# Kernel optimization log

Hardware: AMD Instinct MI355X
Metric: run time of the kernel (lower is better)

Reference implementation:

```python
import jax, jax.numpy as jnp
import numpy as np

N_ITERATIONS = 3  # matches init_kwargs n_iterations


def squash(s):
    # s: [batch, output_caps, output_dim]
    sq = jnp.sum(s * s, axis=2, keepdims=True)          # [b, oc, 1]
    return s * (sq / (1.0 + sq) / jnp.sqrt(sq))


def setup_inputs() -> dict:
    key = jax.random.key(0)
    k_u, = jax.random.split(key, 1)
    batch, ic, oc, od = 128, 2048, 32, 16
    u_predict = jax.random.normal(k_u, (batch, ic, oc, od), dtype=jnp.float32)
    b = jnp.zeros((ic, oc), dtype=jnp.float32)  # routing logit prior, init zeros per torch module
    return {"u_predict": u_predict, "b": b}


def reference(u_predict, b):
    # u_predict: [batch, input_caps, output_caps, output_dim]; b: [input_caps, output_caps]
    batch = u_predict.shape[0]
    c = jax.nn.softmax(b, axis=1)                              # softmax over output_caps (torch implicit dim=1 on 2D)
    s = jnp.einsum('io,biod->bod', c, u_predict)               # weighted sum over input_caps
    v = squash(s)
    b_batch = jnp.broadcast_to(b, (batch,) + b.shape)          # [b, ic, oc]
    for _ in range(N_ITERATIONS):
        b_batch = b_batch + jnp.einsum('biod,bod->bio', u_predict, v)  # agreement
        c = jax.nn.softmax(b_batch, axis=-1)                   # coupling coeffs over output_caps
        s = jnp.einsum('bio,biod->bod', c, u_predict)
        v = squash(s)
    return v
```

## Files before the change

### kernel.cpp

```cpp
#include <hip/hip_runtime.h>
#include <math.h>


namespace {
constexpr int BATCH = 128;
constexpr int IC    = 2048;
constexpr int OC    = 32;
constexpr int ROW   = 512;
constexpr int BPB   = 16;
constexpr int ROWS_PER_BLOCK = IC / BPB;
constexpr int NWAVES = 4;
constexpr int HROW  = ROW / 8;

typedef _Float16 half8 __attribute__((ext_vector_type(8)));
typedef float    f32x4 __attribute__((ext_vector_type(4)));

constexpr size_t OFF_U16    = 0;
constexpr size_t PART_BYTES = (size_t)BATCH * BPB * ROW * 4;
constexpr size_t OFF_P0     = 268435456;
constexpr size_t OFF_P1     = OFF_P0 + PART_BYTES;
constexpr size_t OFF_WA     = OFF_P1 + PART_BYTES;
constexpr size_t OFF_WB     = OFF_WA + 262144;
}

__global__ void __launch_bounds__(256)
pass0_convert(const float* __restrict__ u, const float* __restrict__ blogit,
              _Float16* __restrict__ u16, float* __restrict__ partials)
{
    const int tid = threadIdx.x, lane = tid & 63, wave = tid >> 6;
    const int b = blockIdx.x >> 4, chunk = blockIdx.x & 15;
    const int o = lane >> 1, elem0 = lane * 8;
    const int i_base = chunk * ROWS_PER_BLOCK + wave * 32;

    f32x4 acc0 = {0.f,0.f,0.f,0.f}, acc1 = {0.f,0.f,0.f,0.f};

    const float*  ubase = u   + ((size_t)b * IC + i_base) * ROW + elem0;
    _Float16*     obase = u16 + ((size_t)b * IC + i_base) * ROW + elem0;

#pragma unroll 4
    for (int r = 0; r < 32; ++r) {
        const float* up = ubase + (size_t)r * ROW;
        f32x4 u0 = __builtin_nontemporal_load((const f32x4*)up);
        f32x4 u1 = __builtin_nontemporal_load((const f32x4*)(up + 4));
        float e = __expf(blogit[(i_base + r) * OC + o]);
        float ssum = e;
#pragma unroll
        for (int off = 2; off <= 32; off <<= 1)
            ssum += __shfl_xor(ssum, off, 64);
        const float c = e / ssum;
        acc0 += c * u0;
        acc1 += c * u1;
        half8 h;
        h[0]=(_Float16)u0[0]; h[1]=(_Float16)u0[1]; h[2]=(_Float16)u0[2]; h[3]=(_Float16)u0[3];
        h[4]=(_Float16)u1[0]; h[5]=(_Float16)u1[1]; h[6]=(_Float16)u1[2]; h[7]=(_Float16)u1[3];
        __builtin_nontemporal_store(h, (half8*)(obase + (size_t)r * ROW));
    }

    __shared__ float red[NWAVES * ROW];
    float* my = red + wave * ROW + elem0;
    *(f32x4*)my       = acc0;
    *(f32x4*)(my + 4) = acc1;
    __syncthreads();
    float* dst = partials + (size_t)blockIdx.x * ROW;
    for (int p = tid; p < ROW; p += 256)
        dst[p] = red[p] + red[ROW + p] + red[2*ROW + p] + red[3*ROW + p];
}

template<int IT>
__device__ __forceinline__ void compute_w(const float* __restrict__ part_in,
                                          const float* __restrict__ w_in,
                                          float* __restrict__ w_out,
                                          float* __restrict__ wlds,
                                          int b, int tid, int chunk)
{
    const int p = tid * 2;
    const float* pp = part_in + (size_t)b * (BPB * ROW) + p;
    float s0 = 0.f, s1 = 0.f;
#pragma unroll
    for (int k = 0; k < BPB; ++k) {
        s0 += pp[(size_t)k * ROW];
        s1 += pp[(size_t)k * ROW + 1];
    }
    float sq = s0 * s0 + s1 * s1;
    sq += __shfl_xor(sq, 1, 64);
    sq += __shfl_xor(sq, 2, 64);
    sq += __shfl_xor(sq, 4, 64);
    const float sc = sqrtf(sq) / (1.0f + sq);
    float w0 = s0 * sc, w1 = s1 * sc;
    if (IT > 1) {
        w0 += w_in[b * ROW + p];
        w1 += w_in[b * ROW + p + 1];
    }
    wlds[p]     = w0;
    wlds[p + 1] = w1;
    if (IT < 3 && chunk == 0) {
        w_out[b * ROW + p]     = w0;
        w_out[b * ROW + p + 1] = w1;
    }
}

template<int IT>
__global__ void __launch_bounds__(256)
pass_iter(const _Float16* __restrict__ u16, const float* __restrict__ blogit,
          const float* __restrict__ part_in, const float* __restrict__ w_in,
          float* __restrict__ part_out, float* __restrict__ w_out)
{
    const int tid = threadIdx.x, lane = tid & 63, wave = tid >> 6;
    const int b = blockIdx.x >> 4, chunk = blockIdx.x & 15;
    const int o = lane >> 1, elem0 = lane * 8;
    const int i_base = chunk * ROWS_PER_BLOCK + wave * 32;

    __shared__ float red[NWAVES * ROW];
    __shared__ float wlds[ROW];

    const half8* ubase = (const half8*)(u16 + ((size_t)b * IC + i_base) * ROW + elem0);

    half8 cur[4];
    cur[0] = ubase[0*HROW]; cur[1] = ubase[1*HROW];
    cur[2] = ubase[2*HROW]; cur[3] = ubase[3*HROW];

    compute_w<IT>(part_in, w_in, w_out, wlds, b, tid, chunk);
    __syncthreads();

    const f32x4 w0 = *(const f32x4*)(wlds + elem0);
    const f32x4 w1 = *(const f32x4*)(wlds + elem0 + 4);

    f32x4 acc0 = {0.f,0.f,0.f,0.f}, acc1 = {0.f,0.f,0.f,0.f};

    for (int g = 0; g < 8; ++g) {
        half8 nxt[4];
        if (g < 7) {
            const half8* ptr = ubase + (size_t)(g + 1) * 4 * HROW;
            nxt[0] = ptr[0*HROW]; nxt[1] = ptr[1*HROW];
            nxt[2] = ptr[2*HROW]; nxt[3] = ptr[3*HROW];
        }
        float blg[4];
#pragma unroll
        for (int r = 0; r < 4; ++r)
            blg[r] = blogit[(i_base + g*4 + r) * OC + o];

#pragma unroll
        for (int r = 0; r < 4; ++r) {
            float uf[8];
#pragma unroll
            for (int j = 0; j < 8; ++j) uf[j] = (float)cur[r][j];
            float part = uf[0]*w0[0] + uf[1]*w0[1] + uf[2]*w0[2] + uf[3]*w0[3]
                       + uf[4]*w1[0] + uf[5]*w1[1] + uf[6]*w1[2] + uf[7]*w1[3];
            float bb = blg[r] + part + __shfl_xor(part, 1, 64);
            float e = __expf(bb);
            float ssum = e;
#pragma unroll
            for (int off = 2; off <= 32; off <<= 1)
                ssum += __shfl_xor(ssum, off, 64);
            const float c = e / ssum;
            acc0[0] += c*uf[0]; acc0[1] += c*uf[1]; acc0[2] += c*uf[2]; acc0[3] += c*uf[3];
            acc1[0] += c*uf[4]; acc1[1] += c*uf[5]; acc1[2] += c*uf[6]; acc1[3] += c*uf[7];
        }
#pragma unroll
        for (int r = 0; r < 4; ++r) cur[r] = nxt[r];
    }

    float* my = red + wave * ROW + elem0;
    *(f32x4*)my       = acc0;
    *(f32x4*)(my + 4) = acc1;
    __syncthreads();
    float* dst = part_out + (size_t)blockIdx.x * ROW;
    for (int p = tid; p < ROW; p += 256)
        dst[p] = red[p] + red[ROW + p] + red[2*ROW + p] + red[3*ROW + p];
}

__global__ void __launch_bounds__(256)
reduce_out(const float* __restrict__ partials, float* __restrict__ out)
{
    const int idx = blockIdx.x * 256 + threadIdx.x;
    const int b = idx >> 9, p = idx & 511;
    const float* pp = partials + (size_t)(b * BPB) * ROW + p;
    float s = 0.f;
#pragma unroll
    for (int k = 0; k < BPB; ++k) s += pp[(size_t)k * ROW];
    float sq = s * s;
    sq += __shfl_xor(sq, 1, 64);
    sq += __shfl_xor(sq, 2, 64);
    sq += __shfl_xor(sq, 4, 64);
    sq += __shfl_xor(sq, 8, 64);
    out[idx] = s * (sqrtf(sq) / (1.0f + sq));
}

extern "C" void kernel_launch(void* const* d_in, const int* in_sizes, int n_in,
                              void* d_out, int out_size, void* d_ws, size_t ws_size,
                              hipStream_t stream)
{
    const float* u  = (const float*)d_in[0];
    const float* bl = (const float*)d_in[1];
    float* out = (float*)d_out;

    char* ws = (char*)d_ws;
    _Float16* u16 = (_Float16*)(ws + OFF_U16);
    float* part0  = (float*)(ws + OFF_P0);
    float* part1  = (float*)(ws + OFF_P1);
    float* wA     = (float*)(ws + OFF_WA);
    float* wB     = (float*)(ws + OFF_WB);

    const dim3 blk(256);
    const dim3 gpass(BATCH * BPB);

    pass0_convert<<<gpass, blk, 0, stream>>>(u, bl, u16, part0);
    pass_iter<1> <<<gpass, blk, 0, stream>>>(u16, bl, part0, nullptr, part1, wA);
    pass_iter<2> <<<gpass, blk, 0, stream>>>(u16, bl, part1, wA,      part0, wB);
    pass_iter<3> <<<gpass, blk, 0, stream>>>(u16, bl, part0, wB,      part1, nullptr);
    reduce_out   <<<dim3(BATCH * ROW / 256), blk, 0, stream>>>(part1, out);
}
```

Before: 871.0 us.

## Split batch into halves so fp16 copy of u stays cache-resident across passes

The whole pipeline now runs twice, each time over half the batch (64 samples), and the fp16 conversion store becomes a normal cached store instead of a nontemporal one. The aim is for each half's fp16 working set (about 134 MB) to stay in the large last-level cache, so the three routing passes re-read it from cache rather than HBM. The cost is twice as many kernel launches, each with half the grid (1024 blocks), which may reduce occupancy and add launch and tail overhead.

```diff
diff --git a/kernel.cpp b/kernel.cpp
--- a/kernel.cpp
+++ b/kernel.cpp
@@ -4,6 +4,7 @@
 
 namespace {
 constexpr int BATCH = 128;
+constexpr int BHALF = 64;
 constexpr int IC    = 2048;
 constexpr int OC    = 32;
 constexpr int ROW   = 512;
@@ -25,10 +26,10 @@
 
 __global__ void __launch_bounds__(256)
 pass0_convert(const float* __restrict__ u, const float* __restrict__ blogit,
-              _Float16* __restrict__ u16, float* __restrict__ partials)
+              _Float16* __restrict__ u16, float* __restrict__ partials, int b0)
 {
     const int tid = threadIdx.x, lane = tid & 63, wave = tid >> 6;
-    const int b = blockIdx.x >> 4, chunk = blockIdx.x & 15;
+    const int b = b0 + (blockIdx.x >> 4), chunk = blockIdx.x & 15;
     const int o = lane >> 1, elem0 = lane * 8;
     const int i_base = chunk * ROWS_PER_BLOCK + wave * 32;
 
@@ -53,7 +54,7 @@
         half8 h;
         h[0]=(_Float16)u0[0]; h[1]=(_Float16)u0[1]; h[2]=(_Float16)u0[2]; h[3]=(_Float16)u0[3];
         h[4]=(_Float16)u1[0]; h[5]=(_Float16)u1[1]; h[6]=(_Float16)u1[2]; h[7]=(_Float16)u1[3];
-        __builtin_nontemporal_store(h, (half8*)(obase + (size_t)r * ROW));
+        *(half8*)(obase + (size_t)r * ROW) = h;
     }
 
     __shared__ float red[NWAVES * ROW];
@@ -61,7 +62,7 @@
     *(f32x4*)my       = acc0;
     *(f32x4*)(my + 4) = acc1;
     __syncthreads();
-    float* dst = partials + (size_t)blockIdx.x * ROW;
+    float* dst = partials + ((size_t)b * BPB + chunk) * ROW;
     for (int p = tid; p < ROW; p += 256)
         dst[p] = red[p] + red[ROW + p] + red[2*ROW + p] + red[3*ROW + p];
 }
@@ -103,10 +104,10 @@
 __global__ void __launch_bounds__(256)
 pass_iter(const _Float16* __restrict__ u16, const float* __restrict__ blogit,
           const float* __restrict__ part_in, const float* __restrict__ w_in,
-          float* __restrict__ part_out, float* __restrict__ w_out)
+          float* __restrict__ part_out, float* __restrict__ w_out, int b0)
 {
     const int tid = threadIdx.x, lane = tid & 63, wave = tid >> 6;
-    const int b = blockIdx.x >> 4, chunk = blockIdx.x & 15;
+    const int b = b0 + (blockIdx.x >> 4), chunk = blockIdx.x & 15;
     const int o = lane >> 1, elem0 = lane * 8;
     const int i_base = chunk * ROWS_PER_BLOCK + wave * 32;
 
@@ -164,15 +165,15 @@
     *(f32x4*)my       = acc0;
     *(f32x4*)(my + 4) = acc1;
     __syncthreads();
-    float* dst = part_out + (size_t)blockIdx.x * ROW;
+    float* dst = part_out + ((size_t)b * BPB + chunk) * ROW;
     for (int p = tid; p < ROW; p += 256)
         dst[p] = red[p] + red[ROW + p] + red[2*ROW + p] + red[3*ROW + p];
 }
 
 __global__ void __launch_bounds__(256)
-reduce_out(const float* __restrict__ partials, float* __restrict__ out)
-{
-    const int idx = blockIdx.x * 256 + threadIdx.x;
+reduce_out(const float* __restrict__ partials, float* __restrict__ out, int b0)
+{
+    const int idx = b0 * ROW + blockIdx.x * 256 + threadIdx.x;
     const int b = idx >> 9, p = idx & 511;
     const float* pp = partials + (size_t)(b * BPB) * ROW + p;
     float s = 0.f;
@@ -202,11 +203,15 @@
     float* wB     = (float*)(ws + OFF_WB);
 
     const dim3 blk(256);
-    const dim3 gpass(BATCH * BPB);
-
-    pass0_convert<<<gpass, blk, 0, stream>>>(u, bl, u16, part0);
-    pass_iter<1> <<<gpass, blk, 0, stream>>>(u16, bl, part0, nullptr, part1, wA);
-    pass_iter<2> <<<gpass, blk, 0, stream>>>(u16, bl, part1, wA,      part0, wB);
-    pass_iter<3> <<<gpass, blk, 0, stream>>>(u16, bl, part0, wB,      part1, nullptr);
-    reduce_out   <<<dim3(BATCH * ROW / 256), blk, 0, stream>>>(part1, out);
-}
+    const dim3 gpass(BHALF * BPB);
+    const dim3 gred(BHALF * ROW / 256);
+
+    for (int h = 0; h < 2; ++h) {
+        const int b0 = h * BHALF;
+        pass0_convert<<<gpass, blk, 0, stream>>>(u, bl, u16, part0, b0);
+        pass_iter<1> <<<gpass, blk, 0, stream>>>(u16, bl, part0, nullptr, part1, wA, b0);
+        pass_iter<2> <<<gpass, blk, 0, stream>>>(u16, bl, part1, wA,      part0, wB, b0);
+        pass_iter<3> <<<gpass, blk, 0, stream>>>(u16, bl, part0, wB,      part1, nullptr, b0);
+        reduce_out   <<<gred,  blk, 0, stream>>>(part1, out, b0);
+    }
+}
```

After: 855.5 us. No clear change (-1.8%).
